# Kernel tuning notes

Hardware: AMD Instinct MI355X
Metric: run time of the kernel (lower is better)

## Reference

```python
import jax, jax.numpy as jnp
import numpy as np

M, N, D = 8192, 8192, 256
GAMMA = 1.0 / D  # RBF bandwidth


def setup_inputs() -> dict:
    key = jax.random.key(0)
    k1, k2, k3 = jax.random.split(key, 3)
    Xq = jax.random.normal(k1, (M, D), dtype=jnp.float32)
    Xtrain = jax.random.normal(k2, (N, D), dtype=jnp.float32)
    alpha = jax.random.normal(k3, (N, 1), dtype=jnp.float32)
    return {"Xq": Xq, "Xtrain": Xtrain, "alpha": alpha}


def rbf_kernel(A, B):
    # squared euclidean distances via ||a||^2 + ||b||^2 - 2 a.b  -> [M, N]
    sq_a = jnp.sum(A * A, axis=1, keepdims=True)          # [M,1]
    sq_b = jnp.sum(B * B, axis=1, keepdims=True).T        # [1,N]
    d2 = sq_a + sq_b - 2.0 * jnp.einsum('md,nd->mn', A, B)
    d2 = jnp.maximum(d2, 0.0)
    return jnp.exp(-GAMMA * d2)


def reference(Xq, Xtrain, alpha):
    # forward: kernel(X, self.X) @ self.alpha  -> [M, 1]
    K = rbf_kernel(Xq, Xtrain)
    return K @ alpha
```

## Files before the change

kernel.cpp:

```cpp
#include <hip/hip_runtime.h>
#include <stdint.h>


#define MM 8192
#define NN 8192
#define DD 256
#define GAMMA (1.0f/256.0f)
#define LOG2E 1.44269504088896340736f
#define SCALE_A (2.0f*GAMMA*LOG2E)
#define NEG_G_LOG2E (-GAMMA*LOG2E)

#define NSPLIT 16
#define NPB (NN/NSPLIT)
#define NT_PER (NPB/16)

typedef __bf16 bf16x8 __attribute__((ext_vector_type(8)));
typedef float  f32x4  __attribute__((ext_vector_type(4)));

#define A_OFF  ((size_t)0)
#define B_OFF  ((size_t)4 << 20)
#define W_OFF  ((size_t)8 << 20)
#define EA_OFF (((size_t)8 << 20) + 32768)
#define PART_OFF (((size_t)8 << 20) + 65536)

__device__ __forceinline__ unsigned short f2bf(float f) {
  union { float f; uint32_t u; } x; x.f = f;
  uint32_t u = x.u;
  u += 0x7FFFu + ((u >> 16) & 1u);
  return (unsigned short)(u >> 16);
}
__device__ __forceinline__ uint32_t pack2(float a, float b) {
  return (uint32_t)f2bf(a) | ((uint32_t)f2bf(b) << 16);
}

__global__ __launch_bounds__(256) void prep_kernel(
    const float* __restrict__ Xq, const float* __restrict__ Xt,
    const float* __restrict__ alpha,
    char* __restrict__ Amat, char* __restrict__ Bmat,
    float* __restrict__ w, float* __restrict__ ea)
{
  const int lane = threadIdx.x & 63;
  const int gw = blockIdx.x * 4 + (threadIdx.x >> 6);
  const bool isA = gw < 512;
  const int t = isA ? gw : gw - 512;
  const float* __restrict__ src = isA ? Xq : Xt;
  char* __restrict__ dst = isA ? Amat : Bmat;
  const float sc = isA ? SCALE_A : 1.0f;
  const int n = t * 16 + (lane & 15);
  float ss = 0.f;
#pragma unroll
  for (int r = 0; r < 8; ++r) {
    const int gg = r * 4 + (lane >> 4);
    const float* p = src + (size_t)n * DD + gg * 8;
    const float4 f0 = *(const float4*)p;
    const float4 f1 = *(const float4*)(p + 4);
    ss += f0.x*f0.x + f0.y*f0.y + f0.z*f0.z + f0.w*f0.w
        + f1.x*f1.x + f1.y*f1.y + f1.z*f1.z + f1.w*f1.w;
    uint4 pk;
    pk.x = pack2(f0.x * sc, f0.y * sc); pk.y = pack2(f0.z * sc, f0.w * sc);
    pk.z = pack2(f1.x * sc, f1.y * sc); pk.w = pack2(f1.z * sc, f1.w * sc);
    *(uint4*)(dst + (size_t)t * 8192 + r * 1024 + lane * 16) = pk;
  }
  ss += __shfl_xor(ss, 16, 64);
  ss += __shfl_xor(ss, 32, 64);
  if (lane < 16) {
    if (isA) ea[n] = __builtin_amdgcn_exp2f(NEG_G_LOG2E * ss);
    else     w[n]  = alpha[n] * __builtin_amdgcn_exp2f(NEG_G_LOG2E * ss);
  }
}

__global__ __launch_bounds__(256, 2) void rbf_main(
    const char* __restrict__ Amat, const char* __restrict__ Bmat,
    const float* __restrict__ w, const float* __restrict__ ea,
    float* __restrict__ part)
{
  __shared__ float lds_w[NPB];
  const int tid  = threadIdx.x;
  const int wave = tid >> 6, lane = tid & 63;
  const int quad = lane >> 4, l16 = lane & 15;

  const int b    = blockIdx.x;
  const int xcd  = b & 7, slot = b >> 3;
  const int my   = (xcd & 3) * 8 + (slot & 7);
  const int nx   = (xcd >> 2) * 8 + (slot >> 3);
  const int mt0    = my * 16 + wave * 4;
  const int nt0    = nx * NT_PER;
  const int nbase0 = nx * NPB;

  {
    const float2 wv2 = *(const float2*)(w + nbase0 + tid * 2);
    lds_w[tid * 2]     = wv2.x;
    lds_w[tid * 2 + 1] = wv2.y;
  }

  bf16x8 afrag[4][8];
#pragma unroll
  for (int rt = 0; rt < 4; ++rt)
#pragma unroll
    for (int kc = 0; kc < 8; ++kc) {
      union { uint4 u; bf16x8 v; } cv;
      cv.u = *(const uint4*)(Amat + (size_t)(mt0 + rt) * 8192 + kc * 1024 + lane * 16);
      afrag[rt][kc] = cv.v;
    }

  __syncthreads();

  float outacc[4][4] = {{0,0,0,0},{0,0,0,0},{0,0,0,0},{0,0,0,0}};

  uint4 bufA[8], bufB[8];
  auto loadB = [&](uint4* dst, int ct) {
#pragma unroll
    for (int kc = 0; kc < 8; ++kc)
      dst[kc] = *(const uint4*)(Bmat + (size_t)(nt0 + ct) * 8192 + kc * 1024 + lane * 16);
  };

  const f32x4 fzero = {0.f, 0.f, 0.f, 0.f};
  f32x4 accA[4], accB[4];

  auto mfmaInto = [&](f32x4* acc, const uint4* buf) {
#pragma unroll
    for (int rt = 0; rt < 4; ++rt) acc[rt] = fzero;
#pragma unroll
    for (int kc = 0; kc < 8; ++kc) {
      union { uint4 u; bf16x8 v; } cv; cv.u = buf[kc];
#pragma unroll
      for (int rt = 0; rt < 4; ++rt)
        acc[rt] = __builtin_amdgcn_mfma_f32_16x16x32_bf16(afrag[rt][kc], cv.v, acc[rt], 0, 0, 0);
    }
  };
  auto epi = [&](const f32x4* acc, int ct) {
    const float wv = lds_w[ct * 16 + l16];
#pragma unroll
    for (int rt = 0; rt < 4; ++rt) {
      outacc[rt][0] += wv * __builtin_amdgcn_exp2f(acc[rt][0]);
      outacc[rt][1] += wv * __builtin_amdgcn_exp2f(acc[rt][1]);
      outacc[rt][2] += wv * __builtin_amdgcn_exp2f(acc[rt][2]);
      outacc[rt][3] += wv * __builtin_amdgcn_exp2f(acc[rt][3]);
    }
  };

  loadB(bufA, 0);
  loadB(bufB, 1);
  mfmaInto(accA, bufA);
  for (int ct = 0; ct < NT_PER - 2; ct += 2) {
    loadB(bufA, ct + 2);
    mfmaInto(accB, bufB);
    epi(accA, ct);
    loadB(bufB, ct + 3);
    mfmaInto(accA, bufA);
    epi(accB, ct + 1);
  }
  mfmaInto(accB, bufB);
  epi(accA, NT_PER - 2);
  epi(accB, NT_PER - 1);

#pragma unroll
  for (int rt = 0; rt < 4; ++rt)
#pragma unroll
    for (int i = 0; i < 4; ++i) {
      float v = outacc[rt][i];
      v += __shfl_xor(v, 1, 64);
      v += __shfl_xor(v, 2, 64);
      v += __shfl_xor(v, 4, 64);
      v += __shfl_xor(v, 8, 64);
      if (l16 == 0) {
        const int row = my * 256 + wave * 64 + rt * 16 + quad * 4 + i;
        part[(size_t)nx * MM + row] = ea[row] * v;
      }
    }
}

__global__ __launch_bounds__(256) void reduce_kernel(
    const float* __restrict__ part, float* __restrict__ out)
{
  const int row = blockIdx.x * 256 + threadIdx.x;
  float s = 0.f;
#pragma unroll
  for (int i = 0; i < NSPLIT; ++i) s += part[(size_t)i * MM + row];
  out[row] = s;
}

extern "C" void kernel_launch(void* const* d_in, const int* in_sizes, int n_in,
                              void* d_out, int out_size, void* d_ws, size_t ws_size,
                              hipStream_t stream) {
  const float* Xq    = (const float*)d_in[0];
  const float* Xt    = (const float*)d_in[1];
  const float* alpha = (const float*)d_in[2];
  float* out = (float*)d_out;
  char*  ws  = (char*)d_ws;

  char*  Amat = ws + A_OFF;
  char*  Bmat = ws + B_OFF;
  float* w    = (float*)(ws + W_OFF);
  float* ea   = (float*)(ws + EA_OFF);
  float* part = (float*)(ws + PART_OFF);

  hipLaunchKernelGGL(prep_kernel, dim3(256), dim3(256), 0, stream,
                     Xq, Xt, alpha, Amat, Bmat, w, ea);
  hipLaunchKernelGGL(rbf_main, dim3(512), dim3(256), 0, stream,
                     Amat, Bmat, w, ea, part);
  hipLaunchKernelGGL(reduce_kernel, dim3(MM / 256), dim3(256), 0, stream,
                     part, out);
}
```

Before: 99.40 us.

## Stage B tiles through shared LDS ring and replace reduce kernel with atomics

Each block now loads its B tiles once into a 4-slot shared-memory ring buffer, filled cooperatively with a register-staged prefetch, so the four waves no longer each fetch the same B tile from global memory. It also zeroes the output in the prep kernel and accumulates partial row sums with atomicAdd, which removes the separate reduce kernel launch and the partial-sum buffer. The cost is a __syncthreads per pair of tiles, extra LDS traffic, and float atomics that make the summation order nondeterministic.

Result: slower. 120.6 us (+21.3%).

```diff
diff --git a/kernel.cpp b/kernel.cpp
--- a/kernel.cpp
+++ b/kernel.cpp
@@ -21,7 +21,6 @@
 #define B_OFF  ((size_t)4 << 20)
 #define W_OFF  ((size_t)8 << 20)
 #define EA_OFF (((size_t)8 << 20) + 32768)
-#define PART_OFF (((size_t)8 << 20) + 65536)
 
 __device__ __forceinline__ unsigned short f2bf(float f) {
   union { float f; uint32_t u; } x; x.f = f;
@@ -37,8 +36,11 @@
     const float* __restrict__ Xq, const float* __restrict__ Xt,
     const float* __restrict__ alpha,
     char* __restrict__ Amat, char* __restrict__ Bmat,
-    float* __restrict__ w, float* __restrict__ ea)
+    float* __restrict__ w, float* __restrict__ ea, float* __restrict__ out)
 {
+  const int gi = blockIdx.x * 256 + threadIdx.x;
+  if (gi < MM) out[gi] = 0.f;
+
   const int lane = threadIdx.x & 63;
   const int gw = blockIdx.x * 4 + (threadIdx.x >> 6);
   const bool isA = gw < 512;
@@ -72,9 +74,11 @@
 __global__ __launch_bounds__(256, 2) void rbf_main(
     const char* __restrict__ Amat, const char* __restrict__ Bmat,
     const float* __restrict__ w, const float* __restrict__ ea,
-    float* __restrict__ part)
+    float* __restrict__ out)
 {
   __shared__ float lds_w[NPB];
+  __shared__ uint4 lds_b[4][512];
+
   const int tid  = threadIdx.x;
   const int wave = tid >> 6, lane = tid & 63;
   const int quad = lane >> 4, l16 = lane & 15;
@@ -87,12 +91,30 @@
   const int nt0    = nx * NT_PER;
   const int nbase0 = nx * NPB;
 
+  const uint4* __restrict__ Bm4 = (const uint4*)Bmat;
+
+  uint4 st[4];
+  auto stageL = [&](int t0) {
+#pragma unroll
+    for (int i = 0; i < 2; ++i) {
+      st[i*2+0] = Bm4[(size_t)(nt0 + t0 + i) * 512 + tid];
+      st[i*2+1] = Bm4[(size_t)(nt0 + t0 + i) * 512 + 256 + tid];
+    }
+  };
+  auto stageW = [&](int t0) {
+#pragma unroll
+    for (int i = 0; i < 2; ++i) {
+      lds_b[(t0 + i) & 3][tid]       = st[i*2+0];
+      lds_b[(t0 + i) & 3][256 + tid] = st[i*2+1];
+    }
+  };
+
+  stageL(0);
   {
     const float2 wv2 = *(const float2*)(w + nbase0 + tid * 2);
     lds_w[tid * 2]     = wv2.x;
     lds_w[tid * 2 + 1] = wv2.y;
   }
-
   bf16x8 afrag[4][8];
 #pragma unroll
   for (int rt = 0; rt < 4; ++rt)
@@ -102,57 +124,46 @@
       cv.u = *(const uint4*)(Amat + (size_t)(mt0 + rt) * 8192 + kc * 1024 + lane * 16);
       afrag[rt][kc] = cv.v;
     }
-
+  stageW(0);
+  stageL(2);
   __syncthreads();
 
   float outacc[4][4] = {{0,0,0,0},{0,0,0,0},{0,0,0,0},{0,0,0,0}};
-
-  uint4 bufA[8], bufB[8];
-  auto loadB = [&](uint4* dst, int ct) {
-#pragma unroll
-    for (int kc = 0; kc < 8; ++kc)
-      dst[kc] = *(const uint4*)(Bmat + (size_t)(nt0 + ct) * 8192 + kc * 1024 + lane * 16);
-  };
-
   const f32x4 fzero = {0.f, 0.f, 0.f, 0.f};
-  f32x4 accA[4], accB[4];
-
-  auto mfmaInto = [&](f32x4* acc, const uint4* buf) {
-#pragma unroll
-    for (int rt = 0; rt < 4; ++rt) acc[rt] = fzero;
-#pragma unroll
-    for (int kc = 0; kc < 8; ++kc) {
-      union { uint4 u; bf16x8 v; } cv; cv.u = buf[kc];
-#pragma unroll
-      for (int rt = 0; rt < 4; ++rt)
-        acc[rt] = __builtin_amdgcn_mfma_f32_16x16x32_bf16(afrag[rt][kc], cv.v, acc[rt], 0, 0, 0);
-    }
-  };
-  auto epi = [&](const f32x4* acc, int ct) {
-    const float wv = lds_w[ct * 16 + l16];
-#pragma unroll
-    for (int rt = 0; rt < 4; ++rt) {
-      outacc[rt][0] += wv * __builtin_amdgcn_exp2f(acc[rt][0]);
-      outacc[rt][1] += wv * __builtin_amdgcn_exp2f(acc[rt][1]);
-      outacc[rt][2] += wv * __builtin_amdgcn_exp2f(acc[rt][2]);
-      outacc[rt][3] += wv * __builtin_amdgcn_exp2f(acc[rt][3]);
-    }
-  };
-
-  loadB(bufA, 0);
-  loadB(bufB, 1);
-  mfmaInto(accA, bufA);
-  for (int ct = 0; ct < NT_PER - 2; ct += 2) {
-    loadB(bufA, ct + 2);
-    mfmaInto(accB, bufB);
-    epi(accA, ct);
-    loadB(bufB, ct + 3);
-    mfmaInto(accA, bufA);
-    epi(accB, ct + 1);
-  }
-  mfmaInto(accB, bufB);
-  epi(accA, NT_PER - 2);
-  epi(accB, NT_PER - 1);
+
+  for (int s = 0; s < 16; ++s) {
+    if (s < 15) stageW(2 * s + 2);
+    if (s < 14) stageL(2 * s + 4);
+#pragma unroll
+    for (int half = 0; half < 2; ++half) {
+      const int ct = 2 * s + half;
+      const uint4* bp = &lds_b[ct & 3][0];
+      bf16x8 bf[8];
+#pragma unroll
+      for (int kc = 0; kc < 8; ++kc) {
+        union { uint4 u; bf16x8 v; } cv;
+        cv.u = bp[kc * 64 + lane];
+        bf[kc] = cv.v;
+      }
+      f32x4 acc[4];
+#pragma unroll
+      for (int rt = 0; rt < 4; ++rt) acc[rt] = fzero;
+#pragma unroll
+      for (int kc = 0; kc < 8; ++kc)
+#pragma unroll
+        for (int rt = 0; rt < 4; ++rt)
+          acc[rt] = __builtin_amdgcn_mfma_f32_16x16x32_bf16(afrag[rt][kc], bf[kc], acc[rt], 0, 0, 0);
+      const float wv = lds_w[ct * 16 + l16];
+#pragma unroll
+      for (int rt = 0; rt < 4; ++rt) {
+        outacc[rt][0] += wv * __builtin_amdgcn_exp2f(acc[rt][0]);
+        outacc[rt][1] += wv * __builtin_amdgcn_exp2f(acc[rt][1]);
+        outacc[rt][2] += wv * __builtin_amdgcn_exp2f(acc[rt][2]);
+        outacc[rt][3] += wv * __builtin_amdgcn_exp2f(acc[rt][3]);
+      }
+    }
+    __syncthreads();
+  }
 
 #pragma unroll
   for (int rt = 0; rt < 4; ++rt)
@@ -165,19 +176,9 @@
       v += __shfl_xor(v, 8, 64);
       if (l16 == 0) {
         const int row = my * 256 + wave * 64 + rt * 16 + quad * 4 + i;
-        part[(size_t)nx * MM + row] = ea[row] * v;
+        atomicAdd(&out[row], ea[row] * v);
       }
     }
-}
-
-__global__ __launch_bounds__(256) void reduce_kernel(
-    const float* __restrict__ part, float* __restrict__ out)
-{
-  const int row = blockIdx.x * 256 + threadIdx.x;
-  float s = 0.f;
-#pragma unroll
-  for (int i = 0; i < NSPLIT; ++i) s += part[(size_t)i * MM + row];
-  out[row] = s;
 }
 
 extern "C" void kernel_launch(void* const* d_in, const int* in_sizes, int n_in,
@@ -193,12 +194,9 @@
   char*  Bmat = ws + B_OFF;
   float* w    = (float*)(ws + W_OFF);
   float* ea   = (float*)(ws + EA_OFF);
-  float* part = (float*)(ws + PART_OFF);
 
   hipLaunchKernelGGL(prep_kernel, dim3(256), dim3(256), 0, stream,
-                     Xq, Xt, alpha, Amat, Bmat, w, ea);
+                     Xq, Xt, alpha, Amat, Bmat, w, ea, out);
   hipLaunchKernelGGL(rbf_main, dim3(512), dim3(256), 0, stream,
-                     Amat, Bmat, w, ea, part);
-  hipLaunchKernelGGL(reduce_kernel, dim3(MM / 256), dim3(256), 0, stream,
-                     part, out);
-}
+                     Amat, Bmat, w, ea, out);
+}
```

## Replace partial-sum reduce kernel with atomics, remap block tiles, prioritize MFMA waves

Applied to the files above, without the earlier changes.

Drops the third reduce launch. The prep kernel now zeroes the output and the main kernel atomically adds each split's row contribution into it. The block-to-tile mapping within each XCD is changed so co-resident blocks share A/B tiles differently, and s_setprio raises wave priority around the MFMA loop to interleave better with the exp epilogue. Atomics add contention (16 adders per row) and make the floating-point summation order nondeterministic.

New measurement: 155.2 us. 56.1% more time.

```diff
diff --git a/kernel.cpp b/kernel.cpp
--- a/kernel.cpp
+++ b/kernel.cpp
@@ -21,7 +21,6 @@
 #define B_OFF  ((size_t)4 << 20)
 #define W_OFF  ((size_t)8 << 20)
 #define EA_OFF (((size_t)8 << 20) + 32768)
-#define PART_OFF (((size_t)8 << 20) + 65536)
 
 __device__ __forceinline__ unsigned short f2bf(float f) {
   union { float f; uint32_t u; } x; x.f = f;
@@ -37,8 +36,11 @@
     const float* __restrict__ Xq, const float* __restrict__ Xt,
     const float* __restrict__ alpha,
     char* __restrict__ Amat, char* __restrict__ Bmat,
-    float* __restrict__ w, float* __restrict__ ea)
+    float* __restrict__ w, float* __restrict__ ea, float* __restrict__ out)
 {
+  const int gi = blockIdx.x * 256 + threadIdx.x;
+  if (gi < MM) out[gi] = 0.f;
+
   const int lane = threadIdx.x & 63;
   const int gw = blockIdx.x * 4 + (threadIdx.x >> 6);
   const bool isA = gw < 512;
@@ -72,7 +74,7 @@
 __global__ __launch_bounds__(256, 2) void rbf_main(
     const char* __restrict__ Amat, const char* __restrict__ Bmat,
     const float* __restrict__ w, const float* __restrict__ ea,
-    float* __restrict__ part)
+    float* __restrict__ out)
 {
   __shared__ float lds_w[NPB];
   const int tid  = threadIdx.x;
@@ -81,8 +83,8 @@
 
   const int b    = blockIdx.x;
   const int xcd  = b & 7, slot = b >> 3;
-  const int my   = (xcd & 3) * 8 + (slot & 7);
-  const int nx   = (xcd >> 2) * 8 + (slot >> 3);
+  const int my   = (xcd & 3) * 8 + ((slot >> 5) << 2) + (slot & 3);
+  const int nx   = (xcd >> 2) * 8 + ((slot >> 2) & 7);
   const int mt0    = my * 16 + wave * 4;
   const int nt0    = nx * NT_PER;
   const int nbase0 = nx * NPB;
@@ -120,6 +122,7 @@
   auto mfmaInto = [&](f32x4* acc, const uint4* buf) {
 #pragma unroll
     for (int rt = 0; rt < 4; ++rt) acc[rt] = fzero;
+    __builtin_amdgcn_s_setprio(1);
 #pragma unroll
     for (int kc = 0; kc < 8; ++kc) {
       union { uint4 u; bf16x8 v; } cv; cv.u = buf[kc];
@@ -127,6 +130,7 @@
       for (int rt = 0; rt < 4; ++rt)
         acc[rt] = __builtin_amdgcn_mfma_f32_16x16x32_bf16(afrag[rt][kc], cv.v, acc[rt], 0, 0, 0);
     }
+    __builtin_amdgcn_s_setprio(0);
   };
   auto epi = [&](const f32x4* acc, int ct) {
     const float wv = lds_w[ct * 16 + l16];
@@ -165,19 +169,9 @@
       v += __shfl_xor(v, 8, 64);
       if (l16 == 0) {
         const int row = my * 256 + wave * 64 + rt * 16 + quad * 4 + i;
-        part[(size_t)nx * MM + row] = ea[row] * v;
+        atomicAdd(&out[row], ea[row] * v);
       }
     }
-}
-
-__global__ __launch_bounds__(256) void reduce_kernel(
-    const float* __restrict__ part, float* __restrict__ out)
-{
-  const int row = blockIdx.x * 256 + threadIdx.x;
-  float s = 0.f;
-#pragma unroll
-  for (int i = 0; i < NSPLIT; ++i) s += part[(size_t)i * MM + row];
-  out[row] = s;
 }
 
 extern "C" void kernel_launch(void* const* d_in, const int* in_sizes, int n_in,
@@ -193,12 +187,9 @@
   char*  Bmat = ws + B_OFF;
   float* w    = (float*)(ws + W_OFF);
   float* ea   = (float*)(ws + EA_OFF);
-  float* part = (float*)(ws + PART_OFF);
 
   hipLaunchKernelGGL(prep_kernel, dim3(256), dim3(256), 0, stream,
-                     Xq, Xt, alpha, Amat, Bmat, w, ea);
+                     Xq, Xt, alpha, Amat, Bmat, w, ea, out);
   hipLaunchKernelGGL(rbf_main, dim3(512), dim3(256), 0, stream,
-                     Amat, Bmat, w, ea, part);
-  hipLaunchKernelGGL(reduce_kernel, dim3(MM / 256), dim3(256), 0, stream,
-                     part, out);
+                     Amat, Bmat, w, ea, out);
 }
```
